# Optimization experiments

Measured on AMD Instinct MI355X. Metric: run time of the kernel, lower is better.

The kernel has to match this reference:

```python
import jax, jax.numpy as jnp
import numpy as np

N, C, H, W = 16, 512, 32, 32
NH = 8            # num_heads
HD = C // NH      # head dim c = 64
G = C // 4        # GroupNorm groups = 128
EPS = 1e-5


def conv1x1(X, Wt, b):
    # 1x1 Conv2d == per-pixel linear over channels
    return jnp.einsum('oc,nchw->nohw', Wt, X) + b[None, :, None, None]


def setup_inputs() -> dict:
    key = jax.random.key(0)
    ks = jax.random.split(key, 9)
    s = 0.02
    inp = {
        'X': jax.random.normal(ks[0], (N, C, H, W), jnp.float32),
        'Wq': jax.random.normal(ks[1], (C, C), jnp.float32) * s,
        'bq': jax.random.normal(ks[2], (C,), jnp.float32) * s,
        'Wk': jax.random.normal(ks[3], (C, C), jnp.float32) * s,
        'bk': jax.random.normal(ks[4], (C,), jnp.float32) * s,
        'Wv': jax.random.normal(ks[5], (C, C), jnp.float32) * s,
        'bv': jax.random.normal(ks[6], (C,), jnp.float32) * s,
        'Wo': jax.random.normal(ks[7], (C, C), jnp.float32) * s,
        'bo': jax.random.normal(ks[8], (C,), jnp.float32) * s,
        'gn_w': jnp.ones((C,), jnp.float32),
        'gn_b': jnp.zeros((C,), jnp.float32),
    }
    return inp


def reference(X, Wq, bq, Wk, bk, Wv, bv, Wo, bo, gn_w, gn_b):
    # NOTE: original torch code does  K, Q, V = (Q_conv(X), K_conv(X), V_conv(X))
    # i.e. K gets the Q_conv weights and Q gets the K_conv weights; mirror that.
    K = conv1x1(X, Wq, bq)
    Q = conv1x1(X, Wk, bk)
    V = conv1x1(X, Wv, bv)

    d = H * W
    Kh = K.reshape(N, NH, HD, d)  # [n,h,c,d]
    Qh = Q.reshape(N, NH, HD, d)
    Vh = V.reshape(N, NH, HD, d)

    # softmax-free channel attention: (Q^T K) then V (Q^T K)^T
    A = jnp.einsum('nhcd,nhcD->nhdD', Qh, Kh)   # [n,h,d,d]
    O = jnp.einsum('nhdD,nhcD->nhcd', A, Vh)    # [n,h,c,d]

    O = O.reshape(N, C, H, W)
    O = conv1x1(O, Wo, bo)

    # GroupNorm(G, C) with affine, eps=1e-5
    Og = O.reshape(N, G, C // G, H, W)
    mu = Og.mean(axis=(2, 3, 4), keepdims=True)
    var = Og.var(axis=(2, 3, 4), keepdims=True)
    On = ((Og - mu) * jax.lax.rsqrt(var + EPS)).reshape(N, C, H, W)
    On = On * gn_w[None, :, None, None] + gn_b[None, :, None, None]

    return On + X
```

## Files before the change

### kernel.cpp

```cpp
#include <hip/hip_runtime.h>
#include <hip/hip_bf16.h>

typedef __attribute__((ext_vector_type(8))) short s8v;
typedef __attribute__((ext_vector_type(4))) short s4v;
typedef __attribute__((ext_vector_type(4))) float f32x4;

#define MFMA_BF16 __builtin_amdgcn_mfma_f32_16x16x32_bf16

__device__ inline void gload_lds16(const __hip_bfloat16* g, __hip_bfloat16* l) {
  __builtin_amdgcn_global_load_lds(
      (const __attribute__((address_space(1))) void*)g,
      (__attribute__((address_space(3))) void*)l, 16, 0, 0);
}

__device__ inline short f2bs(float x) {
  __hip_bfloat16 b = __float2bfloat16(x);
  return *reinterpret_cast<short*>(&b);
}

__device__ inline void storeC(float* p, float v) { *p = v; }
__device__ inline void storeC(__hip_bfloat16* p, float v) { *p = __float2bfloat16(v); }

__global__ __launch_bounds__(256) void xt_conv(const float* __restrict__ X,
                                               __hip_bfloat16* __restrict__ XT) {
  __shared__ float tl[64][65];
  const int n = blockIdx.z;
  const int c0 = blockIdx.y * 64, p0 = blockIdx.x * 64;
  const int tid = threadIdx.x;
  const int lr = tid >> 4, lc4 = (tid & 15) * 4;
  const float* Xp = X + ((long)n * 512 + c0) * 1024 + p0;
#pragma unroll
  for (int i = 0; i < 4; ++i) {
    const int ch = i * 16 + lr;
    const float4 v = *(const float4*)&Xp[(long)ch * 1024 + lc4];
    tl[ch][lc4 + 0] = v.x; tl[ch][lc4 + 1] = v.y;
    tl[ch][lc4 + 2] = v.z; tl[ch][lc4 + 3] = v.w;
  }
  __syncthreads();
  __hip_bfloat16* XTp = XT + ((long)n * 1024 + p0) * 512 + c0;
#pragma unroll
  for (int i = 0; i < 4; ++i) {
    const int px = i * 16 + lr;
    s4v o;
#pragma unroll
    for (int e = 0; e < 4; ++e) o[e] = f2bs(tl[lc4 + e][px]);
    *(s4v*)&XTp[(long)px * 512 + lc4] = o;
  }
}

__global__ __launch_bounds__(256) void wconv(const float* __restrict__ Wq,
                                             const float* __restrict__ Wv,
                                             const float* __restrict__ Wk,
                                             const float* __restrict__ Wo,
                                             const float* __restrict__ bq,
                                             const float* __restrict__ bv,
                                             __hip_bfloat16* __restrict__ WA,
                                             __hip_bfloat16* __restrict__ WkT,
                                             __hip_bfloat16* __restrict__ WOb,
                                             float* __restrict__ biasKV) {
  const int i = blockIdx.x * 256 + threadIdx.x;
  WA[i] = __float2bfloat16(Wq[i]);
  WA[262144 + i] = __float2bfloat16(Wv[i]);
  WOb[i] = __float2bfloat16(Wo[i]);
  WkT[i] = __float2bfloat16(Wk[(i & 511) * 512 + (i >> 9)]);
  if (i < 512) { biasKV[i] = bq[i]; biasKV[512 + i] = bv[i]; }
}

template <typename OutT, bool BROW>
__global__ __launch_bounds__(256) void gemm_nt(
    const __hip_bfloat16* __restrict__ A, long strideA,
    const __hip_bfloat16* __restrict__ B, long strideB,
    OutT* __restrict__ C, long strideC, int K, int ldc,
    const float* __restrict__ brow, long strideBrow) {
  A += blockIdx.z * strideA;
  B += blockIdx.z * strideB;
  C += blockIdx.z * strideC;
  const int m0 = blockIdx.y * 128;
  const int n0 = blockIdx.x * 128;
  const int tid = threadIdx.x;
  const int wid = tid >> 6, lane = tid & 63;
  const int wm = wid >> 1, wn = wid & 1;

  __shared__ __hip_bfloat16 As[128 * 64];
  __shared__ __hip_bfloat16 Bs[128 * 64];

  f32x4 acc[4][4] = {};

  const __hip_bfloat16* gA0 = A + (long)(m0 + wid * 32 + (lane >> 3)) * K + (lane & 7) * 8;
  const __hip_bfloat16* gB0 = B + (long)(n0 + wid * 32 + (lane >> 3)) * K + (lane & 7) * 8;

  for (int k0 = 0; k0 < K; k0 += 64) {
#pragma unroll
    for (int t = 0; t < 4; ++t) {
      gload_lds16(gA0 + (long)t * 8 * K + k0, &As[(wid * 32 + t * 8) * 64]);
      gload_lds16(gB0 + (long)t * 8 * K + k0, &Bs[(wid * 32 + t * 8) * 64]);
    }
    __syncthreads();
#pragma unroll
    for (int ks = 0; ks < 2; ++ks) {
      const int koff = ks * 32 + (lane >> 4) * 8;
      s8v a[4], b[4];
#pragma unroll
      for (int i = 0; i < 4; ++i)
        a[i] = *(const s8v*)&As[(wm * 64 + i * 16 + (lane & 15)) * 64 + koff];
#pragma unroll
      for (int j = 0; j < 4; ++j)
        b[j] = *(const s8v*)&Bs[(wn * 64 + j * 16 + (lane & 15)) * 64 + koff];
#pragma unroll
      for (int i = 0; i < 4; ++i)
#pragma unroll
        for (int j = 0; j < 4; ++j)
          acc[i][j] = MFMA_BF16(a[i], b[j], acc[i][j], 0, 0, 0);
    }
    __syncthreads();
  }

  const int cr = (lane >> 4) * 4;
  const int cc = lane & 15;
#pragma unroll
  for (int i = 0; i < 4; ++i) {
#pragma unroll
    for (int r = 0; r < 4; ++r) {
      const int gm = m0 + wm * 64 + i * 16 + cr + r;
      const float rb = BROW ? brow[blockIdx.z * strideBrow + gm] : 0.f;
#pragma unroll
      for (int j = 0; j < 4; ++j) {
        const int gn = n0 + wn * 64 + j * 16 + cc;
        storeC(&C[(long)gm * ldc + gn], acc[i][j][r] + rb);
      }
    }
  }
}

__global__ __launch_bounds__(512) void gemm_vkT(const __hip_bfloat16* __restrict__ V,
                                                const __hip_bfloat16* __restrict__ Kk,
                                                __hip_bfloat16* __restrict__ Mt) {
  const int n = blockIdx.x >> 3, h = blockIdx.x & 7;
  const int tid = threadIdx.x, wid = tid >> 6, lane = tid & 63;
  f32x4 acc[4][4] = {};
  const long colbase = (long)n * 1024 + wid * 128 + (lane >> 4) * 8;
  const __hip_bfloat16* Vb = V + (long)(h * 64 + (lane & 15)) * 16384 + colbase;
  const __hip_bfloat16* Kb = Kk + (long)(h * 64 + (lane & 15)) * 16384 + colbase;
#pragma unroll
  for (int kk = 0; kk < 128; kk += 32) {
    s8v a[4], b[4];
#pragma unroll
    for (int i = 0; i < 4; ++i) a[i] = *(const s8v*)(Vb + (long)i * 16 * 16384 + kk);
#pragma unroll
    for (int j = 0; j < 4; ++j) b[j] = *(const s8v*)(Kb + (long)j * 16 * 16384 + kk);
#pragma unroll
    for (int i = 0; i < 4; ++i)
#pragma unroll
      for (int j = 0; j < 4; ++j) acc[i][j] = MFMA_BF16(a[i], b[j], acc[i][j], 0, 0, 0);
  }
  __shared__ float part[4][4096];
  const int cr = (lane >> 4) * 4, cc = lane & 15;
  if (wid < 4) {
#pragma unroll
    for (int i = 0; i < 4; ++i)
#pragma unroll
      for (int r = 0; r < 4; ++r)
#pragma unroll
        for (int j = 0; j < 4; ++j)
          part[wid][(i * 16 + cr + r) * 64 + j * 16 + cc] = acc[i][j][r];
  }
  __syncthreads();
  if (wid >= 4) {
#pragma unroll
    for (int i = 0; i < 4; ++i)
#pragma unroll
      for (int r = 0; r < 4; ++r)
#pragma unroll
        for (int j = 0; j < 4; ++j)
          part[wid - 4][(i * 16 + cr + r) * 64 + j * 16 + cc] += acc[i][j][r];
  }
  __syncthreads();
  __hip_bfloat16* outp = Mt + ((long)n * 8 + h) * 4096;
  for (int e = tid; e < 4096; e += 512) {
    const float sum = part[0][e] + part[1][e] + part[2][e] + part[3][e];
    outp[(e & 63) * 64 + (e >> 6)] = __float2bfloat16(sum);
  }
}

__global__ __launch_bounds__(256) void wprime_mfma(const __hip_bfloat16* __restrict__ WOb,
                                                   const __hip_bfloat16* __restrict__ Mt,
                                                   __hip_bfloat16* __restrict__ Wp) {
  const int rt = blockIdx.x, h = blockIdx.y, n = blockIdx.z;
  const int tid = threadIdx.x, wid = tid >> 6, lane = tid & 63;
  const int row0 = rt * 256 + wid * 64;
  f32x4 acc[4][4] = {};
  const __hip_bfloat16* Ab =
      WOb + (long)(row0 + (lane & 15)) * 512 + h * 64 + (lane >> 4) * 8;
  const __hip_bfloat16* Bb =
      Mt + (((long)(n * 8 + h)) * 64 + (lane & 15)) * 64 + (lane >> 4) * 8;
#pragma unroll
  for (int ks = 0; ks < 2; ++ks) {
    s8v a[4], b[4];
#pragma unroll
    for (int i = 0; i < 4; ++i) a[i] = *(const s8v*)(Ab + (long)i * 16 * 512 + ks * 32);
#pragma unroll
    for (int j = 0; j < 4; ++j) b[j] = *(const s8v*)(Bb + (long)j * 16 * 64 + ks * 32);
#pragma unroll
    for (int i = 0; i < 4; ++i)
#pragma unroll
      for (int j = 0; j < 4; ++j) acc[i][j] = MFMA_BF16(a[i], b[j], acc[i][j], 0, 0, 0);
  }
  const int cr = (lane >> 4) * 4, cc = lane & 15;
#pragma unroll
  for (int i = 0; i < 4; ++i)
#pragma unroll
    for (int r = 0; r < 4; ++r)
#pragma unroll
      for (int j = 0; j < 4; ++j)
        Wp[((long)n * 512 + (row0 + i * 16 + cr + r)) * 512 + h * 64 + j * 16 + cc] =
            __float2bfloat16(acc[i][j][r]);
}

__global__ __launch_bounds__(256) void bias2k(const __hip_bfloat16* __restrict__ Wp,
                                              const float* __restrict__ bk,
                                              const float* __restrict__ bo,
                                              float* __restrict__ b2) {
  const int r = blockIdx.x * 4 + (threadIdx.x >> 6);
  const int lane = threadIdx.x & 63;
  const s8v w = *(const s8v*)&Wp[(long)r * 512 + lane * 8];
  const float4 k0 = *(const float4*)&bk[lane * 8];
  const float4 k1 = *(const float4*)&bk[lane * 8 + 4];
  const __hip_bfloat16* wb = (const __hip_bfloat16*)&w;
  float s = __bfloat162float(wb[0]) * k0.x + __bfloat162float(wb[1]) * k0.y +
            __bfloat162float(wb[2]) * k0.z + __bfloat162float(wb[3]) * k0.w +
            __bfloat162float(wb[4]) * k1.x + __bfloat162float(wb[5]) * k1.y +
            __bfloat162float(wb[6]) * k1.z + __bfloat162float(wb[7]) * k1.w;
#pragma unroll
  for (int off = 32; off; off >>= 1) s += __shfl_down(s, off);
  if (lane == 0) b2[r] = s + bo[r & 511];
}

__global__ __launch_bounds__(256) void gn_res(const __hip_bfloat16* __restrict__ Y,
                                              const float* __restrict__ X,
                                              const float* __restrict__ gw,
                                              const float* __restrict__ gb,
                                              float* __restrict__ out) {
  const int n = blockIdx.x >> 7, g = blockIdx.x & 127;
  const long base = ((long)n * 512 + g * 4) * 1024;
  const int tid = threadIdx.x;
  float v[16];
  float s = 0.f, s2 = 0.f;
#pragma unroll
  for (int i = 0; i < 2; ++i) {
    const s8v x = *(const s8v*)&Y[base + ((long)(i * 256 + tid)) * 8];
#pragma unroll
    for (int e = 0; e < 8; ++e) {
      const float f = __bfloat162float(((const __hip_bfloat16*)&x)[e]);
      v[i * 8 + e] = f;
      s += f;
      s2 += f * f;
    }
  }
#pragma unroll
  for (int off = 32; off; off >>= 1) {
    s += __shfl_down(s, off);
    s2 += __shfl_down(s2, off);
  }
  __shared__ float rs[8];
  const int wid = tid >> 6, lane = tid & 63;
  if (lane == 0) { rs[wid] = s; rs[4 + wid] = s2; }
  __syncthreads();
  if (tid == 0) {
    const float ts = rs[0] + rs[1] + rs[2] + rs[3];
    const float t2 = rs[4] + rs[5] + rs[6] + rs[7];
    const float mu = ts * (1.f / 4096.f);
    const float var = t2 * (1.f / 4096.f) - mu * mu;
    rs[0] = mu;
    rs[1] = rsqrtf(var + 1e-5f);
  }
  __syncthreads();
  const float mu = rs[0], rstd = rs[1];
#pragma unroll
  for (int i = 0; i < 2; ++i) {
    const int chunk = i * 256 + tid;
    const long e0 = base + (long)chunk * 8;
    const int c = g * 4 + (chunk >> 7);
    const float sc = rstd * gw[c], sh = gb[c];
    const float4 x0 = *(const float4*)&X[e0];
    const float4 x1 = *(const float4*)&X[e0 + 4];
    float4 o0, o1;
    o0.x = (v[i * 8 + 0] - mu) * sc + sh + x0.x;
    o0.y = (v[i * 8 + 1] - mu) * sc + sh + x0.y;
    o0.z = (v[i * 8 + 2] - mu) * sc + sh + x0.z;
    o0.w = (v[i * 8 + 3] - mu) * sc + sh + x0.w;
    o1.x = (v[i * 8 + 4] - mu) * sc + sh + x1.x;
    o1.y = (v[i * 8 + 5] - mu) * sc + sh + x1.y;
    o1.z = (v[i * 8 + 6] - mu) * sc + sh + x1.z;
    o1.w = (v[i * 8 + 7] - mu) * sc + sh + x1.w;
    *(float4*)&out[e0] = o0;
    *(float4*)&out[e0 + 4] = o1;
  }
}

extern "C" void kernel_launch(void* const* d_in, const int* in_sizes, int n_in,
                              void* d_out, int out_size, void* d_ws, size_t ws_size,
                              hipStream_t stream) {
  const float* X  = (const float*)d_in[0];
  const float* Wq = (const float*)d_in[1];
  const float* bq = (const float*)d_in[2];
  const float* Wk = (const float*)d_in[3];
  const float* bk = (const float*)d_in[4];
  const float* Wv = (const float*)d_in[5];
  const float* bv = (const float*)d_in[6];
  const float* Wo = (const float*)d_in[7];
  const float* bo = (const float*)d_in[8];
  const float* gw = (const float*)d_in[9];
  const float* gb = (const float*)d_in[10];
  float* out = (float*)d_out;

  char* ws = (char*)d_ws;
  __hip_bfloat16* XT  = (__hip_bfloat16*)(ws + 0);
  __hip_bfloat16* KV  = (__hip_bfloat16*)(ws + 16777216);
  __hip_bfloat16* Y   = (__hip_bfloat16*)(ws + 16777216);
  __hip_bfloat16* WP  = (__hip_bfloat16*)(ws + 50331648);
  __hip_bfloat16* WPP = (__hip_bfloat16*)(ws + 58720256);
  __hip_bfloat16* Mt  = (__hip_bfloat16*)(ws + 67108864);
  __hip_bfloat16* WA  = (__hip_bfloat16*)(ws + 68157440);
  __hip_bfloat16* WkT = (__hip_bfloat16*)(ws + 69206016);
  __hip_bfloat16* WOb = (__hip_bfloat16*)(ws + 69730304);
  float*          bKV = (float*)(ws + 70254592);
  float*          b2  = (float*)(ws + 70258688);

  xt_conv<<<dim3(16, 8, 16), 256, 0, stream>>>(X, XT);
  wconv<<<1024, 256, 0, stream>>>(Wq, Wv, Wk, Wo, bq, bv, WA, WkT, WOb, bKV);
  gemm_nt<__hip_bfloat16, true><<<dim3(128, 8, 1), 256, 0, stream>>>(
      WA, 0, XT, 0, KV, 0, 512, 16384, bKV, 0);
  gemm_vkT<<<128, 512, 0, stream>>>(KV + (long)512 * 16384, KV, Mt);
  wprime_mfma<<<dim3(2, 8, 16), 256, 0, stream>>>(WOb, Mt, WP);
  bias2k<<<2048, 256, 0, stream>>>(WP, bk, bo, b2);
  gemm_nt<__hip_bfloat16, false><<<dim3(4, 4, 16), 256, 0, stream>>>(
      WP, 262144, WkT, 0, WPP, 262144, 512, 512, nullptr, 0);
  gemm_nt<__hip_bfloat16, true><<<dim3(8, 4, 16), 256, 0, stream>>>(
      WPP, 262144, XT, 524288, Y, 524288, 512, 1024, b2, 512);
  gn_res<<<2048, 256, 0, stream>>>(Y, X, gw, gb, out);
}
```

Before: 117.5 us.

## Fuse weight-chain GEMMs and bias into one kernel, merge prep launches

Replaces the three kernels that built W' = Wo·blockdiag(M), its bias projection with bk, and W'·Wk^T with a single wchain kernel. Per head it stages Wo, WkT and Mt tiles in LDS, forms the intermediate product in swizzled LDS and accumulates straight into the final WPP tile, so the intermediate WP array never goes through global memory. The bias is computed by the c0==0 blocks. The X transpose and weight conversion are also merged into one launch via an extra grid slice. In exchange the intermediate is recomputed for each of the four column tiles, and the bias-computing blocks do extra work.

After: 117.2 us. No clear change (-0.3%).

```diff
diff --git a/kernel.cpp b/kernel.cpp
--- a/kernel.cpp
+++ b/kernel.cpp
@@ -21,12 +21,35 @@
 __device__ inline void storeC(float* p, float v) { *p = v; }
 __device__ inline void storeC(__hip_bfloat16* p, float v) { *p = __float2bfloat16(v); }
 
-__global__ __launch_bounds__(256) void xt_conv(const float* __restrict__ X,
-                                               __hip_bfloat16* __restrict__ XT) {
+__global__ __launch_bounds__(256) void prep(const float* __restrict__ X,
+                                            __hip_bfloat16* __restrict__ XT,
+                                            const float* __restrict__ Wq,
+                                            const float* __restrict__ Wv,
+                                            const float* __restrict__ Wk,
+                                            const float* __restrict__ Wo,
+                                            const float* __restrict__ bq,
+                                            const float* __restrict__ bv,
+                                            __hip_bfloat16* __restrict__ WA,
+                                            __hip_bfloat16* __restrict__ WkT,
+                                            __hip_bfloat16* __restrict__ WOb,
+                                            float* __restrict__ biasKV) {
+  const int tid = threadIdx.x;
+  if (blockIdx.z == 16) {
+    const int blk = blockIdx.y * 16 + blockIdx.x;
+#pragma unroll
+    for (int t = 0; t < 8; ++t) {
+      const int i = (blk * 8 + t) * 256 + tid;
+      WA[i] = __float2bfloat16(Wq[i]);
+      WA[262144 + i] = __float2bfloat16(Wv[i]);
+      WOb[i] = __float2bfloat16(Wo[i]);
+      WkT[i] = __float2bfloat16(Wk[(i & 511) * 512 + (i >> 9)]);
+      if (i < 512) { biasKV[i] = bq[i]; biasKV[512 + i] = bv[i]; }
+    }
+    return;
+  }
   __shared__ float tl[64][65];
   const int n = blockIdx.z;
   const int c0 = blockIdx.y * 64, p0 = blockIdx.x * 64;
-  const int tid = threadIdx.x;
   const int lr = tid >> 4, lc4 = (tid & 15) * 4;
   const float* Xp = X + ((long)n * 512 + c0) * 1024 + p0;
 #pragma unroll
@@ -46,24 +69,6 @@
     for (int e = 0; e < 4; ++e) o[e] = f2bs(tl[lc4 + e][px]);
     *(s4v*)&XTp[(long)px * 512 + lc4] = o;
   }
-}
-
-__global__ __launch_bounds__(256) void wconv(const float* __restrict__ Wq,
-                                             const float* __restrict__ Wv,
-                                             const float* __restrict__ Wk,
-                                             const float* __restrict__ Wo,
-                                             const float* __restrict__ bq,
-                                             const float* __restrict__ bv,
-                                             __hip_bfloat16* __restrict__ WA,
-                                             __hip_bfloat16* __restrict__ WkT,
-                                             __hip_bfloat16* __restrict__ WOb,
-                                             float* __restrict__ biasKV) {
-  const int i = blockIdx.x * 256 + threadIdx.x;
-  WA[i] = __float2bfloat16(Wq[i]);
-  WA[262144 + i] = __float2bfloat16(Wv[i]);
-  WOb[i] = __float2bfloat16(Wo[i]);
-  WkT[i] = __float2bfloat16(Wk[(i & 511) * 512 + (i >> 9)]);
-  if (i < 512) { biasKV[i] = bq[i]; biasKV[512 + i] = bv[i]; }
 }
 
 template <typename OutT, bool BROW>
@@ -182,57 +187,125 @@
   }
 }
 
-__global__ __launch_bounds__(256) void wprime_mfma(const __hip_bfloat16* __restrict__ WOb,
-                                                   const __hip_bfloat16* __restrict__ Mt,
-                                                   __hip_bfloat16* __restrict__ Wp) {
-  const int rt = blockIdx.x, h = blockIdx.y, n = blockIdx.z;
-  const int tid = threadIdx.x, wid = tid >> 6, lane = tid & 63;
-  const int row0 = rt * 256 + wid * 64;
-  f32x4 acc[4][4] = {};
-  const __hip_bfloat16* Ab =
-      WOb + (long)(row0 + (lane & 15)) * 512 + h * 64 + (lane >> 4) * 8;
-  const __hip_bfloat16* Bb =
-      Mt + (((long)(n * 8 + h)) * 64 + (lane & 15)) * 64 + (lane >> 4) * 8;
-#pragma unroll
-  for (int ks = 0; ks < 2; ++ks) {
-    s8v a[4], b[4];
-#pragma unroll
-    for (int i = 0; i < 4; ++i) a[i] = *(const s8v*)(Ab + (long)i * 16 * 512 + ks * 32);
-#pragma unroll
-    for (int j = 0; j < 4; ++j) b[j] = *(const s8v*)(Bb + (long)j * 16 * 64 + ks * 32);
-#pragma unroll
-    for (int i = 0; i < 4; ++i)
-#pragma unroll
-      for (int j = 0; j < 4; ++j) acc[i][j] = MFMA_BF16(a[i], b[j], acc[i][j], 0, 0, 0);
-  }
-  const int cr = (lane >> 4) * 4, cc = lane & 15;
-#pragma unroll
-  for (int i = 0; i < 4; ++i)
-#pragma unroll
-    for (int r = 0; r < 4; ++r)
-#pragma unroll
-      for (int j = 0; j < 4; ++j)
-        Wp[((long)n * 512 + (row0 + i * 16 + cr + r)) * 512 + h * 64 + j * 16 + cc] =
-            __float2bfloat16(acc[i][j][r]);
-}
-
-__global__ __launch_bounds__(256) void bias2k(const __hip_bfloat16* __restrict__ Wp,
+__global__ __launch_bounds__(256) void wchain(const __hip_bfloat16* __restrict__ WOb,
+                                              const __hip_bfloat16* __restrict__ WkT,
+                                              const __hip_bfloat16* __restrict__ Mt,
                                               const float* __restrict__ bk,
                                               const float* __restrict__ bo,
-                                              float* __restrict__ b2) {
-  const int r = blockIdx.x * 4 + (threadIdx.x >> 6);
-  const int lane = threadIdx.x & 63;
-  const s8v w = *(const s8v*)&Wp[(long)r * 512 + lane * 8];
-  const float4 k0 = *(const float4*)&bk[lane * 8];
-  const float4 k1 = *(const float4*)&bk[lane * 8 + 4];
-  const __hip_bfloat16* wb = (const __hip_bfloat16*)&w;
-  float s = __bfloat162float(wb[0]) * k0.x + __bfloat162float(wb[1]) * k0.y +
-            __bfloat162float(wb[2]) * k0.z + __bfloat162float(wb[3]) * k0.w +
-            __bfloat162float(wb[4]) * k1.x + __bfloat162float(wb[5]) * k1.y +
-            __bfloat162float(wb[6]) * k1.z + __bfloat162float(wb[7]) * k1.w;
-#pragma unroll
-  for (int off = 32; off; off >>= 1) s += __shfl_down(s, off);
-  if (lane == 0) b2[r] = s + bo[r & 511];
+                                              __hip_bfloat16* __restrict__ WPP,
+                                              float* __restrict__ b2out) {
+  const int c0 = blockIdx.x * 128, o0 = blockIdx.y * 128, n = blockIdx.z;
+  const int tid = threadIdx.x, wid = tid >> 6, lane = tid & 63;
+  const int wm = wid >> 1, wn = wid & 1;
+  const int cr = (lane >> 4) * 4, cc = lane & 15;
+
+  __shared__ __hip_bfloat16 WoS[128 * 64];
+  __shared__ __hip_bfloat16 WkS[128 * 64];
+  __shared__ __hip_bfloat16 MtS[64 * 64];
+  __shared__ __hip_bfloat16 W1S[128 * 64];
+  __shared__ float bkS[512];
+
+  if (tid < 128) *(float4*)&bkS[tid * 4] = *(const float4*)&bk[tid * 4];
+
+  f32x4 acc2[4][4] = {};
+  float bacc = 0.f;
+  const int r8 = lane >> 3, b8 = (lane & 7) * 8;
+
+  for (int h = 0; h < 8; ++h) {
+#pragma unroll
+    for (int t = 0; t < 4; ++t) {
+      const int row = wid * 32 + t * 8;
+      gload_lds16(WOb + (long)(o0 + row + r8) * 512 + h * 64 + b8, &WoS[row * 64]);
+      gload_lds16(WkT + (long)(c0 + row + r8) * 512 + h * 64 + b8, &WkS[row * 64]);
+    }
+    {
+      const __hip_bfloat16* mg = Mt + ((long)n * 8 + h) * 4096;
+      gload_lds16(mg + wid * 512 + lane * 8, &MtS[wid * 512]);
+      gload_lds16(mg + 2048 + wid * 512 + lane * 8, &MtS[2048 + wid * 512]);
+    }
+    __syncthreads();
+
+    f32x4 acc1[2][4] = {};
+#pragma unroll
+    for (int ks = 0; ks < 2; ++ks) {
+      const int ko = ks * 32 + (lane >> 4) * 8;
+      s8v aj[2], bw[4];
+#pragma unroll
+      for (int i = 0; i < 2; ++i)
+        aj[i] = *(const s8v*)&MtS[(wn * 32 + i * 16 + cc) * 64 + ko];
+#pragma unroll
+      for (int t = 0; t < 4; ++t)
+        bw[t] = *(const s8v*)&WoS[(wm * 64 + t * 16 + cc) * 64 + ko];
+#pragma unroll
+      for (int i = 0; i < 2; ++i)
+#pragma unroll
+        for (int t = 0; t < 4; ++t)
+          acc1[i][t] = MFMA_BF16(aj[i], bw[t], acc1[i][t], 0, 0, 0);
+    }
+#pragma unroll
+    for (int i = 0; i < 2; ++i)
+#pragma unroll
+      for (int t = 0; t < 4; ++t) {
+        const int o = wm * 64 + t * 16 + cc;
+        const int jb = wn * 32 + i * 16 + cr;
+        s4v p;
+#pragma unroll
+        for (int r = 0; r < 4; ++r) p[r] = f2bs(acc1[i][t][r]);
+        *(s4v*)((char*)W1S + ((o * 128 + jb * 2) ^ ((o & 7) << 4))) = p;
+      }
+    __syncthreads();
+
+#pragma unroll
+    for (int ks = 0; ks < 2; ++ks) {
+      const int ko = ks * 32 + (lane >> 4) * 8;
+      s8v a2[4], bw[4];
+#pragma unroll
+      for (int i = 0; i < 4; ++i) {
+        const int o = wm * 64 + i * 16 + cc;
+        a2[i] = *(const s8v*)((char*)W1S + ((o * 128 + ko * 2) ^ ((o & 7) << 4)));
+      }
+#pragma unroll
+      for (int t = 0; t < 4; ++t)
+        bw[t] = *(const s8v*)&WkS[(wn * 64 + t * 16 + cc) * 64 + ko];
+#pragma unroll
+      for (int i = 0; i < 4; ++i)
+#pragma unroll
+        for (int t = 0; t < 4; ++t)
+          acc2[i][t] = MFMA_BF16(a2[i], bw[t], acc2[i][t], 0, 0, 0);
+    }
+
+    if (c0 == 0) {
+      const int o = tid >> 1, half = tid & 1;
+      float s = 0.f;
+#pragma unroll
+      for (int q = 0; q < 4; ++q) {
+        const int jb = half * 64 + q * 16;
+        const s8v w = *(const s8v*)((char*)W1S + ((o * 128 + jb) ^ ((o & 7) << 4)));
+        const __hip_bfloat16* wb = (const __hip_bfloat16*)&w;
+#pragma unroll
+        for (int e = 0; e < 8; ++e)
+          s += __bfloat162float(wb[e]) * bkS[h * 64 + half * 32 + q * 8 + e];
+      }
+      bacc += s;
+    }
+    __syncthreads();
+  }
+
+#pragma unroll
+  for (int i = 0; i < 4; ++i)
+#pragma unroll
+    for (int r = 0; r < 4; ++r)
+#pragma unroll
+      for (int t = 0; t < 4; ++t)
+        WPP[((long)n * 512 + o0 + wm * 64 + i * 16 + cr + r) * 512 +
+            c0 + wn * 64 + t * 16 + cc] = __float2bfloat16(acc2[i][t][r]);
+  if (c0 == 0) {
+    const float tot = bacc + __shfl_xor(bacc, 1);
+    if ((tid & 1) == 0) {
+      const int o = tid >> 1;
+      b2out[n * 512 + o0 + o] = tot + bo[o0 + o];
+    }
+  }
 }
 
 __global__ __launch_bounds__(256) void gn_res(const __hip_bfloat16* __restrict__ Y,
@@ -317,7 +390,6 @@
   __hip_bfloat16* XT  = (__hip_bfloat16*)(ws + 0);
   __hip_bfloat16* KV  = (__hip_bfloat16*)(ws + 16777216);
   __hip_bfloat16* Y   = (__hip_bfloat16*)(ws + 16777216);
-  __hip_bfloat16* WP  = (__hip_bfloat16*)(ws + 50331648);
   __hip_bfloat16* WPP = (__hip_bfloat16*)(ws + 58720256);
   __hip_bfloat16* Mt  = (__hip_bfloat16*)(ws + 67108864);
   __hip_bfloat16* WA  = (__hip_bfloat16*)(ws + 68157440);
@@ -326,15 +398,12 @@
   float*          bKV = (float*)(ws + 70254592);
   float*          b2  = (float*)(ws + 70258688);
 
-  xt_conv<<<dim3(16, 8, 16), 256, 0, stream>>>(X, XT);
-  wconv<<<1024, 256, 0, stream>>>(Wq, Wv, Wk, Wo, bq, bv, WA, WkT, WOb, bKV);
+  prep<<<dim3(16, 8, 17), 256, 0, stream>>>(X, XT, Wq, Wv, Wk, Wo, bq, bv,
+                                            WA, WkT, WOb, bKV);
   gemm_nt<__hip_bfloat16, true><<<dim3(128, 8, 1), 256, 0, stream>>>(
       WA, 0, XT, 0, KV, 0, 512, 16384, bKV, 0);
   gemm_vkT<<<128, 512, 0, stream>>>(KV + (long)512 * 16384, KV, Mt);
-  wprime_mfma<<<dim3(2, 8, 16), 256, 0, stream>>>(WOb, Mt, WP);
-  bias2k<<<2048, 256, 0, stream>>>(WP, bk, bo, b2);
-  gemm_nt<__hip_bfloat16, false><<<dim3(4, 4, 16), 256, 0, stream>>>(
-      WP, 262144, WkT, 0, WPP, 262144, 512, 512, nullptr, 0);
+  wchain<<<dim3(4, 4, 16), 256, 0, stream>>>(WOb, WkT, Mt, bk, bo, WPP, b2);
   gemm_nt<__hip_bfloat16, true><<<dim3(8, 4, 16), 256, 0, stream>>>(
       WPP, 262144, XT, 524288, Y, 524288, 512, 1024, b2, 512);
   gn_res<<<2048, 256, 0, stream>>>(Y, X, gw, gb, out);
```
